# Optimization experiments

Hardware: AMD Instinct MI355X
Metric: run time of the kernel (lower is better)

## Reference

```python
import jax, jax.numpy as jnp
import numpy as np

B, C, H, W = 4, 256, 64, 64
G = 32          # GroupNorm groups
EPS = 1e-6


def setup_inputs() -> dict:
    key = jax.random.key(0)
    ks = jax.random.split(key, 6)
    inp = {
        "x": jax.random.normal(ks[0], (B, C, H, W), dtype=jnp.float32),
        "gamma": jnp.ones((C,), jnp.float32),
        "beta": jnp.zeros((C,), jnp.float32),
        "wq": jax.random.normal(ks[1], (C, C), jnp.float32) * 0.02,
        "bq": jnp.zeros((C,), jnp.float32),
        "wk": jax.random.normal(ks[2], (C, C), jnp.float32) * 0.02,
        "bk": jnp.zeros((C,), jnp.float32),
        "wv": jax.random.normal(ks[3], (C, C), jnp.float32) * 0.02,
        "bv": jnp.zeros((C,), jnp.float32),
        "wp": jax.random.normal(ks[4], (C, C), jnp.float32) * 0.02,
        "bp": jnp.zeros((C,), jnp.float32),
    }
    return inp


def _group_norm(x, gamma, beta):
    b, c, h, w = x.shape
    xs = x.reshape(b, G, c // G, h, w)
    mu = xs.mean(axis=(2, 3, 4), keepdims=True)
    var = xs.var(axis=(2, 3, 4), keepdims=True)  # biased, matches torch GroupNorm
    xn = ((xs - mu) * jax.lax.rsqrt(var + EPS)).reshape(b, c, h, w)
    return xn * gamma[None, :, None, None] + beta[None, :, None, None]


def _conv1x1(s, w, bias):
    # 1x1 conv == per-pixel channel matmul
    return jnp.einsum('oc,bchw->bohw', w, s) + bias[None, :, None, None]


def reference(x, gamma, beta, wq, bq, wk, bk, wv, bv, wp, bp):
    b, c, h, w = x.shape
    s = _group_norm(x, gamma, beta)
    q = _conv1x1(s, wq, bq).reshape(b, c, h * w)  # [B, C, N]
    k = _conv1x1(s, wk, bk).reshape(b, c, h * w)
    v = _conv1x1(s, wv, bv).reshape(b, c, h * w)
    # scores[b,i,j] = sum_c q[b,c,i] k[b,c,j], scaled by C^-1/2
    scores = jnp.einsum('bci,bcj->bij', q, k) * (c ** -0.5)
    attn = jax.nn.softmax(scores, axis=2)
    # h_[b,c,i] = sum_j v[b,c,j] attn[b,i,j]
    h_ = jnp.einsum('bij,bcj->bci', attn, v).reshape(b, c, h, w)
    h_ = _conv1x1(h_, wp, bp)
    return x + h_
```

## Files before the change

### kernel.cpp

```cpp
#include <hip/hip_runtime.h>

#define BB 4
#define CCH 256
#define NPIX 4096
#define EPS 1e-6f

typedef __attribute__((ext_vector_type(8))) short bf16x8;
typedef __attribute__((ext_vector_type(4))) float f32x4;
typedef __attribute__((ext_vector_type(16))) float f32x16;

__device__ __forceinline__ unsigned short f2bf(float f) {
    return (unsigned short)((__float_as_uint(f) + 0x8000u) >> 16);
}
__device__ __forceinline__ float bf2f(unsigned short h) {
    return __uint_as_float((unsigned)h << 16);
}
__device__ __forceinline__ void gl2lds16(const void* g, void* l) {
    __builtin_amdgcn_global_load_lds(
        (const __attribute__((address_space(1))) unsigned int*)g,
        (__attribute__((address_space(3))) unsigned int*)l, 16, 0, 0);
}

__global__ __launch_bounds__(256) void gn_stats(
    const float* __restrict__ x, float2* __restrict__ pst,
    const float* __restrict__ wq, const float* __restrict__ wk,
    const float* __restrict__ wv, const float* __restrict__ wp,
    unsigned short* __restrict__ wb) {
    int bid = blockIdx.x;
    int t = threadIdx.x;
    if (bid >= 256) {
        int e = (bid - 256) * 256 + t;
        const float* srcs[4] = {wp, wq, wk, wv};
#pragma unroll
        for (int m = 0; m < 4; ++m) {
            float4 v = ((const float4*)srcs[m])[e];
            ushort4 hh;
            hh.x = f2bf(v.x); hh.y = f2bf(v.y);
            hh.z = f2bf(v.z); hh.w = f2bf(v.w);
            *(ushort4*)(wb + (size_t)m * 65536 + (size_t)e * 4) = hh;
        }
        return;
    }
    int b = bid >> 6, g = (bid >> 1) & 31, h = bid & 1;
    const float4* x4 = (const float4*)(x + (size_t)(b * CCH + g * 8) * NPIX);
    float s = 0.f, ss = 0.f;
    for (int e = h * 4096 + t; e < h * 4096 + 4096; e += 256) {
        float4 v = x4[e];
        s += v.x + v.y + v.z + v.w;
        ss += v.x * v.x + v.y * v.y + v.z * v.z + v.w * v.w;
    }
    __shared__ float rs[256], rss[256];
    rs[t] = s; rss[t] = ss;
    __syncthreads();
    for (int off = 128; off > 0; off >>= 1) {
        if (t < (unsigned)off) {
            rs[t] += rs[t + off];
            rss[t] += rss[t + off];
        }
        __syncthreads();
    }
    if (t == 0) pst[bid] = make_float2(rs[0], rss[0]);
}

__global__ __launch_bounds__(256) void gn_norm(
    const float* __restrict__ x, const float2* __restrict__ pst,
    const float* __restrict__ gamma, const float* __restrict__ beta,
    unsigned short* __restrict__ sb) {
    int bid = blockIdx.x;
    int b = bid >> 6, g = (bid >> 1) & 31, h = bid & 1;
    float2 p0 = pst[bid & ~1];
    float2 p1 = pst[bid | 1];
    const float inv = 1.0f / (float)(8 * NPIX);
    float m = (p0.x + p1.x) * inv;
    float var = (p0.y + p1.y) * inv - m * m;
    float rstd = rsqrtf(var + EPS);
    float scale[8], shift[8];
#pragma unroll
    for (int ci = 0; ci < 8; ++ci) {
        float ga = gamma[g * 8 + ci], be = beta[g * 8 + ci];
        scale[ci] = rstd * ga;
        shift[ci] = be - m * scale[ci];
    }
    const float4* x4 = (const float4*)(x + (size_t)(b * CCH + g * 8) * NPIX);
#pragma unroll 1
    for (int r = 0; r < 2; ++r) {
        int pq = h * 512 + r * 256 + threadIdx.x;
        __align__(16) unsigned short hh[4][8];
#pragma unroll
        for (int ci = 0; ci < 8; ++ci) {
            float4 v = x4[ci * 1024 + pq];
            hh[0][ci] = f2bf(v.x * scale[ci] + shift[ci]);
            hh[1][ci] = f2bf(v.y * scale[ci] + shift[ci]);
            hh[2][ci] = f2bf(v.z * scale[ci] + shift[ci]);
            hh[3][ci] = f2bf(v.w * scale[ci] + shift[ci]);
        }
        size_t base = ((size_t)(b * NPIX + pq * 4) << 8) + g * 8;
#pragma unroll
        for (int p = 0; p < 4; ++p)
            *(uint4*)(sb + base + (size_t)p * 256) = *(const uint4*)hh[p];
    }
}

__global__ __launch_bounds__(256) void qkv_mfma(
    const unsigned short* __restrict__ sb, const unsigned short* __restrict__ wb,
    const float* __restrict__ bq, const float* __restrict__ bk,
    const float* __restrict__ bv,
    unsigned short* __restrict__ qT, unsigned short* __restrict__ kT,
    unsigned short* __restrict__ vB) {
    __shared__ __align__(16) char lds[34816];
    const int tid = threadIdx.x, lane = tid & 63, w = tid >> 6;
    const int ln15 = lane & 15, q = lane >> 4;
    const int n0 = blockIdx.x * 128;
    const int co0 = blockIdx.y * 128;
    const int z = blockIdx.z;
    const unsigned short* wm = wb + (size_t)(z + 1) * 65536;
    const float* bias = (z == 0) ? bq : (z == 1) ? bk : bv;

    f32x4 acc[2][8];
#pragma unroll
    for (int i2 = 0; i2 < 2; ++i2)
#pragma unroll
        for (int nf = 0; nf < 8; ++nf) {
            acc[i2][nf][0] = 0.f; acc[i2][nf][1] = 0.f;
            acc[i2][nf][2] = 0.f; acc[i2][nf][3] = 0.f;
        }

#pragma unroll 1
    for (int kt = 0; kt < 4; ++kt) {
#pragma unroll
        for (int r = 0; r < 4; ++r) {
            int gch = r * 256 + tid;
            int row = gch >> 3, sidx = gch & 7;
            int cc = sidx ^ (row & 7);
            gl2lds16(sb + ((size_t)(n0 + row) << 8) + kt * 64 + cc * 8,
                     &lds[r * 4096 + w * 1024]);
            gl2lds16(wm + ((size_t)(co0 + row) << 8) + kt * 64 + cc * 8,
                     &lds[16384 + r * 4096 + w * 1024]);
        }
        __syncthreads();
#pragma unroll
        for (int kk = 0; kk < 2; ++kk) {
            int kc = kk * 4 + q;
            bf16x8 af[2], bf[8];
#pragma unroll
            for (int i2 = 0; i2 < 2; ++i2) {
                int row = w * 32 + i2 * 16 + ln15;
                af[i2] = *(const bf16x8*)&lds[row * 128 + ((kc ^ (row & 7)) << 4)];
            }
#pragma unroll
            for (int nf = 0; nf < 8; ++nf) {
                int row = nf * 16 + ln15;
                bf[nf] = *(const bf16x8*)&lds[16384 + row * 128 + ((kc ^ (row & 7)) << 4)];
            }
#pragma unroll
            for (int i2 = 0; i2 < 2; ++i2)
#pragma unroll
                for (int nf = 0; nf < 8; ++nf)
                    acc[i2][nf] = __builtin_amdgcn_mfma_f32_16x16x32_bf16(
                        af[i2], bf[nf], acc[i2][nf], 0, 0, 0);
        }
        __syncthreads();
    }

    float bias_l[8];
#pragma unroll
    for (int nf = 0; nf < 8; ++nf) bias_l[nf] = bias[co0 + nf * 16 + ln15];
    const float scl = (z == 0) ? 0.0625f : 1.0f;
    unsigned short* T = (unsigned short*)lds;
    if (z < 2) {
#pragma unroll
        for (int i2 = 0; i2 < 2; ++i2)
#pragma unroll
            for (int nf = 0; nf < 8; ++nf)
#pragma unroll
                for (int r = 0; r < 4; ++r) {
                    int n_l = w * 32 + i2 * 16 + q * 4 + r;
                    int co_l = nf * 16 + ln15;
                    T[n_l * 136 + co_l] = f2bf((acc[i2][nf][r] + bias_l[nf]) * scl);
                }
    } else {
#pragma unroll
        for (int i2 = 0; i2 < 2; ++i2)
#pragma unroll
            for (int nf = 0; nf < 8; ++nf)
#pragma unroll
                for (int r = 0; r < 4; ++r) {
                    int n_l = w * 32 + i2 * 16 + q * 4 + r;
                    int co_l = nf * 16 + ln15;
                    T[co_l * 136 + n_l] = f2bf(acc[i2][nf][r] + bias_l[nf]);
                }
    }
    __syncthreads();
    int row = tid >> 1, half = tid & 1;
    const uint4* src = (const uint4*)&T[row * 136 + half * 64];
    uint4* dst;
    if (z < 2) {
        unsigned short* qk = (z == 0) ? qT : kT;
        dst = (uint4*)(qk + ((size_t)(n0 + row) << 8) + co0 + half * 64);
    } else {
        int b2 = n0 >> 12, pix0 = n0 & 4095;
        dst = (uint4*)(vB + ((size_t)(b2 * CCH + co0 + row) << 12) + pix0 + half * 64);
    }
#pragma unroll
    for (int u = 0; u < 8; ++u) dst[u] = src[u];
}

__global__ __launch_bounds__(512, 2) void attn_mfma(
    const unsigned short* __restrict__ qT, const unsigned short* __restrict__ kT,
    const unsigned short* __restrict__ vB,
    unsigned short* __restrict__ pO, float* __restrict__ pml) {
    __shared__ __align__(16) char lds[81920];
    const int tid = threadIdx.x, lane = tid & 63, w = tid >> 6;
    const int l31 = lane & 31, lh = lane >> 5;
    const int bx = blockIdx.x;
    const int xk = bx & 7;
    const int b = xk >> 1, jqhi = xk & 1;
    const int outer = bx >> 3;
    const int jqlo = outer & 1, itile = outer >> 1;
    const int i0 = itile * 128;
    const int jbase = (jqhi * 2 + jqlo) * 1024;
    const size_t nb = (size_t)b * NPIX;
    const int iqb = (w >> 1) * 32;
    const int jh = w & 1, jwb = jh * 32;
    const int ipb = (w & 1) * 64;
    const int cqb = (w >> 1) * 64;

#pragma unroll
    for (int t = 0; t < 8; ++t) {
        int gch = (w * 8 + t) * 64 + lane;
        int row = gch >> 5, sc = gch & 31;
        int cc = sc ^ (row & 7);
        gl2lds16(qT + ((nb + i0 + row) << 8) + cc * 8, &lds[(w * 8 + t) * 1024]);
    }
    __syncthreads();
    bf16x8 qf[16];
    {
        int row = iqb + l31;
#pragma unroll
        for (int kc = 0; kc < 16; ++kc) {
            int sc = kc * 2 + lh;
            qf[kc] = *(const bf16x8*)&lds[row * 512 + ((sc ^ (row & 7)) << 4)];
        }
    }
    __syncthreads();

    f32x16 O[2][2];
#pragma unroll
    for (int ig = 0; ig < 2; ++ig)
#pragma unroll
        for (int cg = 0; cg < 2; ++cg)
#pragma unroll
            for (int r = 0; r < 16; ++r) O[ig][cg][r] = 0.f;
    float l_acc[16];
#pragma unroll
    for (int r = 0; r < 16; ++r) l_acc[r] = 0.f;

    {
        const int j0 = jbase;
#pragma unroll
        for (int t = 0; t < 4; ++t) {
            int gch = (w * 4 + t) * 64 + lane;
            int row = gch >> 5, sc = gch & 31;
            int cc = sc ^ (row & 7);
            gl2lds16(kT + ((nb + j0 + row) << 8) + cc * 8, &lds[(w * 4 + t) * 1024]);
        }
#pragma unroll
        for (int t = 0; t < 4; ++t) {
            int gch = (w * 4 + t) * 64 + lane;
            int c = gch >> 3, sv = gch & 7;
            int jc = sv ^ (c & 7);
            gl2lds16(vB + ((size_t)(b * CCH + c) << 12) + j0 + jc * 8,
                     &lds[32768 + (w * 4 + t) * 1024]);
        }
    }

#pragma unroll 1
    for (int jt = 0; jt < 16; ++jt) {
        asm volatile("s_waitcnt vmcnt(4)" ::: "memory");
        __builtin_amdgcn_s_barrier();

        f32x16 S0, S1;
#pragma unroll
        for (int r = 0; r < 16; ++r) { S0[r] = 0.f; S1[r] = 0.f; }
        __builtin_amdgcn_s_setprio(1);
        {
            int krow = jwb + l31;
            int ksw = krow * 512;
#pragma unroll
            for (int kc = 0; kc < 8; ++kc) {
                int sc0 = (2 * kc) * 2 + lh;
                int sc1 = (2 * kc + 1) * 2 + lh;
                bf16x8 k0 = *(const bf16x8*)&lds[ksw + ((sc0 ^ (krow & 7)) << 4)];
                bf16x8 k1 = *(const bf16x8*)&lds[ksw + ((sc1 ^ (krow & 7)) << 4)];
                S0 = __builtin_amdgcn_mfma_f32_32x32x16_bf16(qf[2 * kc], k0, S0, 0, 0, 0);
                S1 = __builtin_amdgcn_mfma_f32_32x32x16_bf16(qf[2 * kc + 1], k1, S1, 0, 0, 0);
            }
        }
        __builtin_amdgcn_s_setprio(0);

        asm volatile("" ::: "memory");
        __builtin_amdgcn_s_barrier();
        if (jt < 15) {
            const int j0n = jbase + (jt + 1) * 64;
#pragma unroll
            for (int t = 0; t < 4; ++t) {
                int gch = (w * 4 + t) * 64 + lane;
                int row = gch >> 5, sc = gch & 31;
                int cc = sc ^ (row & 7);
                gl2lds16(kT + ((nb + j0n + row) << 8) + cc * 8,
                         &lds[(w * 4 + t) * 1024]);
            }
        }

        {
            int col = jwb + l31;
            int chs = (col >> 3) << 4;
            int cof = (col & 7) << 1;
#pragma unroll
            for (int r = 0; r < 16; ++r) {
                float p = __expf(S0[r] + S1[r]);
                l_acc[r] += p;
                int row = iqb + (r & 3) + 8 * (r >> 2) + 4 * lh;
                *(unsigned short*)&lds[65536 + row * 128 +
                    (chs ^ ((row & 7) << 4)) + cof] = f2bf(p);
            }
        }
        asm volatile("s_waitcnt lgkmcnt(0)" ::: "memory");
        __builtin_amdgcn_sched_barrier(0);

        if (jt < 15) {
            asm volatile("s_waitcnt vmcnt(4)" ::: "memory");
        } else {
            asm volatile("s_waitcnt vmcnt(0)" ::: "memory");
        }
        __builtin_amdgcn_s_barrier();

        __builtin_amdgcn_s_setprio(1);
        {
            int pr0 = ipb + l31, pr1 = ipb + 32 + l31;
            int vc0 = cqb + l31, vc1 = cqb + 32 + l31;
#pragma unroll
            for (int kc = 0; kc < 4; ++kc) {
                int pc = kc * 2 + lh;
                bf16x8 pf0 = *(const bf16x8*)&lds[65536 + pr0 * 128 + ((pc ^ (pr0 & 7)) << 4)];
                bf16x8 pf1 = *(const bf16x8*)&lds[65536 + pr1 * 128 + ((pc ^ (pr1 & 7)) << 4)];
                bf16x8 vf0 = *(const bf16x8*)&lds[32768 + vc0 * 128 + ((pc ^ (vc0 & 7)) << 4)];
                bf16x8 vf1 = *(const bf16x8*)&lds[32768 + vc1 * 128 + ((pc ^ (vc1 & 7)) << 4)];
                O[0][0] = __builtin_amdgcn_mfma_f32_32x32x16_bf16(pf0, vf0, O[0][0], 0, 0, 0);
                O[0][1] = __builtin_amdgcn_mfma_f32_32x32x16_bf16(pf0, vf1, O[0][1], 0, 0, 0);
                O[1][0] = __builtin_amdgcn_mfma_f32_32x32x16_bf16(pf1, vf0, O[1][0], 0, 0, 0);
                O[1][1] = __builtin_amdgcn_mfma_f32_32x32x16_bf16(pf1, vf1, O[1][1], 0, 0, 0);
            }
        }
        __builtin_amdgcn_s_setprio(0);

        asm volatile("" ::: "memory");
        __builtin_amdgcn_s_barrier();
        if (jt < 15) {
            const int j0n = jbase + (jt + 1) * 64;
#pragma unroll
            for (int t = 0; t < 4; ++t) {
                int gch = (w * 4 + t) * 64 + lane;
                int c = gch >> 3, sv = gch & 7;
                int jc = sv ^ (c & 7);
                gl2lds16(vB + ((size_t)(b * CCH + c) << 12) + j0n + jc * 8,
                         &lds[32768 + (w * 4 + t) * 1024]);
            }
        }
    }

    size_t pbase = (size_t)bx * (128 * 256);
#pragma unroll
    for (int ig = 0; ig < 2; ++ig)
#pragma unroll
        for (int cg = 0; cg < 2; ++cg)
#pragma unroll
            for (int r = 0; r < 16; ++r) {
                int i = ipb + ig * 32 + (r & 3) + 8 * (r >> 2) + 4 * lh;
                int c = cqb + cg * 32 + l31;
                pO[pbase + i * 256 + c] = f2bf(O[ig][cg][r]);
            }
#pragma unroll
    for (int r = 0; r < 16; ++r) {
        float l = l_acc[r];
        l += __shfl_xor(l, 1);
        l += __shfl_xor(l, 2);
        l += __shfl_xor(l, 4);
        l += __shfl_xor(l, 8);
        l += __shfl_xor(l, 16);
        if (l31 == 0) {
            int row = iqb + (r & 3) + 8 * (r >> 2) + 4 * lh;
            pml[bx * 256 + jh * 128 + row] = l;
        }
    }
}

__global__ __launch_bounds__(256) void attn_merge(
    const unsigned short* __restrict__ pO, const float* __restrict__ pml,
    unsigned short* __restrict__ hN) {
    int bid = blockIdx.x;
    int b = bid & 3, itile = (bid >> 2) & 31, ih = (bid >> 7) & 1;
    int base = itile * 16 + b * 2;
    const int offs[4] = {0, 1, 8, 9};
    __shared__ float fs[64];
    int t = threadIdx.x;
    if (t < 64) {
        float l = 0.f;
#pragma unroll
        for (int s = 0; s < 4; ++s) {
            int px = (base + offs[s]) * 256 + ih * 64 + t;
            l += pml[px] + pml[px + 128];
        }
        fs[t] = 1.0f / l;
    }
    __syncthreads();
    int i = t >> 2, cq = t & 3;
    float f = fs[i];
    int row = ih * 64 + i;
    size_t nrow = ((size_t)(b * NPIX + itile * 128 + row)) << 8;
#pragma unroll
    for (int p = 0; p < 16; ++p) {
        int c = p * 16 + cq * 4;
        float o0 = 0.f, o1 = 0.f, o2 = 0.f, o3 = 0.f;
#pragma unroll
        for (int s = 0; s < 4; ++s) {
            ushort4 a = *(const ushort4*)&pO[(size_t)(base + offs[s]) * 32768 + row * 256 + c];
            o0 += bf2f(a.x); o1 += bf2f(a.y); o2 += bf2f(a.z); o3 += bf2f(a.w);
        }
        ushort4 h;
        h.x = f2bf(o0 * f); h.y = f2bf(o1 * f);
        h.z = f2bf(o2 * f); h.w = f2bf(o3 * f);
        *(ushort4*)&hN[nrow + c] = h;
    }
}

__global__ __launch_bounds__(256) void proj_mfma(
    const unsigned short* __restrict__ hN, const unsigned short* __restrict__ wb,
    const float* __restrict__ bp, const float* __restrict__ x,
    float* __restrict__ out) {
    __shared__ __align__(16) char lds[34816];
    const int tid = threadIdx.x, lane = tid & 63, w = tid >> 6;
    const int ln15 = lane & 15, q = lane >> 4;
    const int n0 = blockIdx.x * 128;
    const int co0 = blockIdx.y * 128;

    f32x4 acc[2][8];
#pragma unroll
    for (int i2 = 0; i2 < 2; ++i2)
#pragma unroll
        for (int nf = 0; nf < 8; ++nf) {
            acc[i2][nf][0] = 0.f; acc[i2][nf][1] = 0.f;
            acc[i2][nf][2] = 0.f; acc[i2][nf][3] = 0.f;
        }

#pragma unroll 1
    for (int kt = 0; kt < 4; ++kt) {
#pragma unroll
        for (int r = 0; r < 4; ++r) {
            int gch = r * 256 + tid;
            int row = gch >> 3, sidx = gch & 7;
            int cc = sidx ^ (row & 7);
            gl2lds16(hN + ((size_t)(n0 + row) << 8) + kt * 64 + cc * 8,
                     &lds[r * 4096 + w * 1024]);
            gl2lds16(wb + ((size_t)(co0 + row) << 8) + kt * 64 + cc * 8,
                     &lds[16384 + r * 4096 + w * 1024]);
        }
        __syncthreads();
#pragma unroll
        for (int kk = 0; kk < 2; ++kk) {
            int kc = kk * 4 + q;
            bf16x8 af[2], bf[8];
#pragma unroll
            for (int i2 = 0; i2 < 2; ++i2) {
                int row = w * 32 + i2 * 16 + ln15;
                af[i2] = *(const bf16x8*)&lds[row * 128 + ((kc ^ (row & 7)) << 4)];
            }
#pragma unroll
            for (int nf = 0; nf < 8; ++nf) {
                int row = nf * 16 + ln15;
                bf[nf] = *(const bf16x8*)&lds[16384 + row * 128 + ((kc ^ (row & 7)) << 4)];
            }
#pragma unroll
            for (int i2 = 0; i2 < 2; ++i2)
#pragma unroll
                for (int nf = 0; nf < 8; ++nf)
                    acc[i2][nf] = __builtin_amdgcn_mfma_f32_16x16x32_bf16(
                        af[i2], bf[nf], acc[i2][nf], 0, 0, 0);
        }
        __syncthreads();
    }

    unsigned short* T = (unsigned short*)lds;
#pragma unroll
    for (int i2 = 0; i2 < 2; ++i2)
#pragma unroll
        for (int nf = 0; nf < 8; ++nf)
#pragma unroll
            for (int r = 0; r < 4; ++r) {
                int n_l = w * 32 + i2 * 16 + q * 4 + r;
                int co_l = nf * 16 + ln15;
                T[co_l * 136 + n_l] = f2bf(acc[i2][nf][r]);
            }
    __syncthreads();
    int row = tid >> 1, half = tid & 1;
    int b2 = n0 >> 12, pix0 = n0 & 4095;
    float br = bp[co0 + row];
    size_t gidx = (((size_t)(b2 * CCH + co0 + row)) << 12) + pix0 + half * 64;
    const unsigned short* trow = &T[row * 136 + half * 64];
#pragma unroll
    for (int u = 0; u < 16; ++u) {
        float4 xv = *(const float4*)&x[gidx + u * 4];
        ushort4 tv = *(const ushort4*)&trow[u * 4];
        float4 o;
        o.x = xv.x + br + bf2f(tv.x);
        o.y = xv.y + br + bf2f(tv.y);
        o.z = xv.z + br + bf2f(tv.z);
        o.w = xv.w + br + bf2f(tv.w);
        *(float4*)&out[gidx + u * 4] = o;
    }
}

extern "C" void kernel_launch(void* const* d_in, const int* in_sizes, int n_in,
                              void* d_out, int out_size, void* d_ws, size_t ws_size,
                              hipStream_t stream) {
    const float* x     = (const float*)d_in[0];
    const float* gamma = (const float*)d_in[1];
    const float* beta  = (const float*)d_in[2];
    const float* wq    = (const float*)d_in[3];
    const float* bq    = (const float*)d_in[4];
    const float* wk    = (const float*)d_in[5];
    const float* bk    = (const float*)d_in[6];
    const float* wv    = (const float*)d_in[7];
    const float* bv    = (const float*)d_in[8];
    const float* wp    = (const float*)d_in[9];
    const float* bp    = (const float*)d_in[10];
    float* out = (float*)d_out;

    char* p = (char*)d_ws;
    unsigned short* sb  = (unsigned short*)p; p += 8388608;
    unsigned short* hN  = sb;
    unsigned short* wb  = (unsigned short*)p; p += 524288;
    unsigned short* pO  = (unsigned short*)p; p += 33554432;
    float*          pml = (float*)p;          p += 524288;
    float2*         pst = (float2*)p;         p += 4096;
    unsigned short* qT  = (unsigned short*)p; p += 8388608;
    unsigned short* kT  = (unsigned short*)p; p += 8388608;
    unsigned short* vB  = (unsigned short*)p;

    gn_stats<<<320, 256, 0, stream>>>(x, pst, wq, wk, wv, wp, wb);
    gn_norm<<<256, 256, 0, stream>>>(x, pst, gamma, beta, sb);
    qkv_mfma<<<dim3(128, 2, 3), 256, 0, stream>>>(sb, wb, bq, bk, bv, qT, kT, vB);
    attn_mfma<<<512, 512, 0, stream>>>(qT, kT, vB, pO, pml);
    attn_merge<<<256, 256, 0, stream>>>(pO, pml, hN);
    proj_mfma<<<dim3(128, 2), 256, 0, stream>>>(hN, wb, bp, x, out);
}
```

Baseline: 230.3 us.

## Double-buffer K/V tiles in attention and halve the key-dimension split

```diff
diff --git a/kernel.cpp b/kernel.cpp
--- a/kernel.cpp
+++ b/kernel.cpp
@@ -205,20 +205,19 @@
     for (int u = 0; u < 8; ++u) dst[u] = src[u];
 }
 
-__global__ __launch_bounds__(512, 2) void attn_mfma(
+__global__ __launch_bounds__(512, 1) void attn_mfma(
     const unsigned short* __restrict__ qT, const unsigned short* __restrict__ kT,
     const unsigned short* __restrict__ vB,
     unsigned short* __restrict__ pO, float* __restrict__ pml) {
-    __shared__ __align__(16) char lds[81920];
+    __shared__ __align__(16) char lds[147456];
     const int tid = threadIdx.x, lane = tid & 63, w = tid >> 6;
     const int l31 = lane & 31, lh = lane >> 5;
     const int bx = blockIdx.x;
     const int xk = bx & 7;
-    const int b = xk >> 1, jqhi = xk & 1;
-    const int outer = bx >> 3;
-    const int jqlo = outer & 1, itile = outer >> 1;
+    const int b = xk >> 1, bjh = xk & 1;
+    const int itile = bx >> 3;
     const int i0 = itile * 128;
-    const int jbase = (jqhi * 2 + jqlo) * 1024;
+    const int jbase = bjh * 2048;
     const size_t nb = (size_t)b * NPIX;
     const int iqb = (w >> 1) * 32;
     const int jh = w & 1, jwb = jh * 32;
@@ -270,12 +269,17 @@
             int c = gch >> 3, sv = gch & 7;
             int jc = sv ^ (c & 7);
             gl2lds16(vB + ((size_t)(b * CCH + c) << 12) + j0 + jc * 8,
-                     &lds[32768 + (w * 4 + t) * 1024]);
+                     &lds[65536 + (w * 4 + t) * 1024]);
         }
     }
 
 #pragma unroll 1
-    for (int jt = 0; jt < 16; ++jt) {
+    for (int jt = 0; jt < 32; ++jt) {
+        const int kb_ = (jt & 1) * 32768;
+        const int vb_ = 65536 + (jt & 1) * 32768;
+        const int kbn = ((jt + 1) & 1) * 32768;
+        const int vbn = 65536 + ((jt + 1) & 1) * 32768;
+
         asm volatile("s_waitcnt vmcnt(4)" ::: "memory");
         __builtin_amdgcn_s_barrier();
 
@@ -285,7 +289,7 @@
         __builtin_amdgcn_s_setprio(1);
         {
             int krow = jwb + l31;
-            int ksw = krow * 512;
+            int ksw = kb_ + krow * 512;
 #pragma unroll
             for (int kc = 0; kc < 8; ++kc) {
                 int sc0 = (2 * kc) * 2 + lh;
@@ -298,9 +302,25 @@
         }
         __builtin_amdgcn_s_setprio(0);
 
-        asm volatile("" ::: "memory");
+        {
+            int col = jwb + l31;
+            int chs = (col >> 3) << 4;
+            int cof = (col & 7) << 1;
+#pragma unroll
+            for (int r = 0; r < 16; ++r) {
+                float p = __expf(S0[r] + S1[r]);
+                l_acc[r] += p;
+                int row = iqb + (r & 3) + 8 * (r >> 2) + 4 * lh;
+                *(unsigned short*)&lds[131072 + row * 128 +
+                    (chs ^ ((row & 7) << 4)) + cof] = f2bf(p);
+            }
+        }
+        asm volatile("s_waitcnt lgkmcnt(0)" ::: "memory");
+        __builtin_amdgcn_sched_barrier(0);
+        asm volatile("s_waitcnt vmcnt(0)" ::: "memory");
         __builtin_amdgcn_s_barrier();
-        if (jt < 15) {
+
+        if (jt < 31) {
             const int j0n = jbase + (jt + 1) * 64;
 #pragma unroll
             for (int t = 0; t < 4; ++t) {
@@ -308,32 +328,9 @@
                 int row = gch >> 5, sc = gch & 31;
                 int cc = sc ^ (row & 7);
                 gl2lds16(kT + ((nb + j0n + row) << 8) + cc * 8,
-                         &lds[(w * 4 + t) * 1024]);
-            }
-        }
-
-        {
-            int col = jwb + l31;
-            int chs = (col >> 3) << 4;
-            int cof = (col & 7) << 1;
-#pragma unroll
-            for (int r = 0; r < 16; ++r) {
-                float p = __expf(S0[r] + S1[r]);
-                l_acc[r] += p;
-                int row = iqb + (r & 3) + 8 * (r >> 2) + 4 * lh;
-                *(unsigned short*)&lds[65536 + row * 128 +
-                    (chs ^ ((row & 7) << 4)) + cof] = f2bf(p);
-            }
-        }
-        asm volatile("s_waitcnt lgkmcnt(0)" ::: "memory");
-        __builtin_amdgcn_sched_barrier(0);
-
-        if (jt < 15) {
-            asm volatile("s_waitcnt vmcnt(4)" ::: "memory");
-        } else {
-            asm volatile("s_waitcnt vmcnt(0)" ::: "memory");
-        }
-        __builtin_amdgcn_s_barrier();
+                         &lds[kbn + (w * 4 + t) * 1024]);
+            }
+        }
 
         __builtin_amdgcn_s_setprio(1);
         {
@@ -342,10 +339,10 @@
 #pragma unroll
             for (int kc = 0; kc < 4; ++kc) {
                 int pc = kc * 2 + lh;
-                bf16x8 pf0 = *(const bf16x8*)&lds[65536 + pr0 * 128 + ((pc ^ (pr0 & 7)) << 4)];
-                bf16x8 pf1 = *(const bf16x8*)&lds[65536 + pr1 * 128 + ((pc ^ (pr1 & 7)) << 4)];
-                bf16x8 vf0 = *(const bf16x8*)&lds[32768 + vc0 * 128 + ((pc ^ (vc0 & 7)) << 4)];
-                bf16x8 vf1 = *(const bf16x8*)&lds[32768 + vc1 * 128 + ((pc ^ (vc1 & 7)) << 4)];
+                bf16x8 pf0 = *(const bf16x8*)&lds[131072 + pr0 * 128 + ((pc ^ (pr0 & 7)) << 4)];
+                bf16x8 pf1 = *(const bf16x8*)&lds[131072 + pr1 * 128 + ((pc ^ (pr1 & 7)) << 4)];
+                bf16x8 vf0 = *(const bf16x8*)&lds[vb_ + vc0 * 128 + ((pc ^ (vc0 & 7)) << 4)];
+                bf16x8 vf1 = *(const bf16x8*)&lds[vb_ + vc1 * 128 + ((pc ^ (vc1 & 7)) << 4)];
                 O[0][0] = __builtin_amdgcn_mfma_f32_32x32x16_bf16(pf0, vf0, O[0][0], 0, 0, 0);
                 O[0][1] = __builtin_amdgcn_mfma_f32_32x32x16_bf16(pf0, vf1, O[0][1], 0, 0, 0);
                 O[1][0] = __builtin_amdgcn_mfma_f32_32x32x16_bf16(pf1, vf0, O[1][0], 0, 0, 0);
@@ -354,9 +351,7 @@
         }
         __builtin_amdgcn_s_setprio(0);
 
-        asm volatile("" ::: "memory");
-        __builtin_amdgcn_s_barrier();
-        if (jt < 15) {
+        if (jt < 31) {
             const int j0n = jbase + (jt + 1) * 64;
 #pragma unroll
             for (int t = 0; t < 4; ++t) {
@@ -364,7 +359,7 @@
                 int c = gch >> 3, sv = gch & 7;
                 int jc = sv ^ (c & 7);
                 gl2lds16(vB + ((size_t)(b * CCH + c) << 12) + j0n + jc * 8,
-                         &lds[32768 + (w * 4 + t) * 1024]);
+                         &lds[vbn + (w * 4 + t) * 1024]);
             }
         }
     }
@@ -400,15 +395,14 @@
     unsigned short* __restrict__ hN) {
     int bid = blockIdx.x;
     int b = bid & 3, itile = (bid >> 2) & 31, ih = (bid >> 7) & 1;
-    int base = itile * 16 + b * 2;
-    const int offs[4] = {0, 1, 8, 9};
+    int base = itile * 8 + b * 2;
     __shared__ float fs[64];
     int t = threadIdx.x;
     if (t < 64) {
         float l = 0.f;
 #pragma unroll
-        for (int s = 0; s < 4; ++s) {
-            int px = (base + offs[s]) * 256 + ih * 64 + t;
+        for (int s = 0; s < 2; ++s) {
+            int px = (base + s) * 256 + ih * 64 + t;
             l += pml[px] + pml[px + 128];
         }
         fs[t] = 1.0f / l;
@@ -423,8 +417,8 @@
         int c = p * 16 + cq * 4;
         float o0 = 0.f, o1 = 0.f, o2 = 0.f, o3 = 0.f;
 #pragma unroll
-        for (int s = 0; s < 4; ++s) {
-            ushort4 a = *(const ushort4*)&pO[(size_t)(base + offs[s]) * 32768 + row * 256 + c];
+        for (int s = 0; s < 2; ++s) {
+            ushort4 a = *(const ushort4*)&pO[(size_t)(base + s) * 32768 + row * 256 + c];
             o0 += bf2f(a.x); o1 += bf2f(a.y); o2 += bf2f(a.z); o3 += bf2f(a.w);
         }
         ushort4 h;
@@ -540,8 +534,8 @@
     unsigned short* sb  = (unsigned short*)p; p += 8388608;
     unsigned short* hN  = sb;
     unsigned short* wb  = (unsigned short*)p; p += 524288;
-    unsigned short* pO  = (unsigned short*)p; p += 33554432;
-    float*          pml = (float*)p;          p += 524288;
+    unsigned short* pO  = (unsigned short*)p; p += 16777216;
+    float*          pml = (float*)p;          p += 262144;
     float2*         pst = (float2*)p;         p += 4096;
     unsigned short* qT  = (unsigned short*)p; p += 8388608;
     unsigned short* kT  = (unsigned short*)p; p += 8388608;
@@ -550,7 +544,7 @@
     gn_stats<<<320, 256, 0, stream>>>(x, pst, wq, wk, wv, wp, wb);
     gn_norm<<<256, 256, 0, stream>>>(x, pst, gamma, beta, sb);
     qkv_mfma<<<dim3(128, 2, 3), 256, 0, stream>>>(sb, wb, bq, bk, bv, qT, kT, vB);
-    attn_mfma<<<512, 512, 0, stream>>>(qT, kT, vB, pO, pml);
+    attn_mfma<<<256, 512, 0, stream>>>(qT, kT, vB, pO, pml);
     attn_merge<<<256, 256, 0, stream>>>(pO, pml, hN);
     proj_mfma<<<dim3(128, 2), 256, 0, stream>>>(hN, wb, bp, x, out);
 }
```

New measurement: 215.4 us (median of 2 runs). 6.5% less time.
